# Performance work log

Hardware: AMD Instinct MI355X
Metric: run time of the kernel (lower is better)

## Reference

```python
import jax, jax.numpy as jnp
import numpy as np

# Module constants (match init_kwargs / DCNv4 defaults)
N, C, H, W = 4, 256, 128, 128
G = 4                       # DCNv4 default group
KS = 3                      # kernel_size
K = KS * KS                 # 9 sampling points per group
Cg = C // G                 # channels per group
PAD_OFF = int(np.ceil(G * K * 3 / 8) * 8)  # 112, padded offset_mask dim
EPS = 1e-5                  # BatchNorm2d eps


def setup_inputs() -> dict:
    key = jax.random.key(0)
    ks = jax.random.split(key, 6)
    s = 0.05
    return {
        "x": jax.random.normal(ks[0], (N, C, H, W), jnp.float32),
        "conv_w": jax.random.normal(ks[1], (C, C, 1, 1), jnp.float32) * s,
        "bn1_gamma": jnp.ones((C,), jnp.float32),
        "bn1_beta": jnp.zeros((C,), jnp.float32),
        "bn1_mean": jnp.zeros((C,), jnp.float32),
        "bn1_var": jnp.ones((C,), jnp.float32),
        "value_w": jax.random.normal(ks[2], (C, C), jnp.float32) * s,
        "value_b": jnp.zeros((C,), jnp.float32),
        "offset_w": jax.random.normal(ks[3], (PAD_OFF, C), jnp.float32) * s,
        "offset_b": jnp.zeros((PAD_OFF,), jnp.float32),
        "out_w": jax.random.normal(ks[4], (C, C), jnp.float32) * s,
        "out_b": jnp.zeros((C,), jnp.float32),
        "bn2_gamma": jnp.ones((C,), jnp.float32),
        "bn2_beta": jnp.zeros((C,), jnp.float32),
        "bn2_mean": jnp.zeros((C,), jnp.float32),
        "bn2_var": jnp.ones((C,), jnp.float32),
    }


def _bilinear(v, lh, lw):
    """Bilinear sample v:(N,H,W,G,Cg) at float locs lh/lw:(N,H,W,G); zero outside."""
    n, h, w, g, c = v.shape
    h0 = jnp.floor(lh)
    w0 = jnp.floor(lw)
    dh = lh - h0
    dw = lw - w0
    h0i = h0.astype(jnp.int32)
    w0i = w0.astype(jnp.int32)
    vf = v.reshape(n, h * w, g, c)

    def gather(hh, ww):
        valid = (hh >= 0) & (hh < h) & (ww >= 0) & (ww < w)
        idx = jnp.clip(hh, 0, h - 1) * w + jnp.clip(ww, 0, w - 1)
        out = jnp.take_along_axis(vf, idx.reshape(n, h * w, g)[..., None], axis=1)
        return out.reshape(n, h, w, g, c) * valid[..., None].astype(v.dtype)

    w00 = (1 - dh) * (1 - dw)
    w01 = (1 - dh) * dw
    w10 = dh * (1 - dw)
    w11 = dh * dw
    return (gather(h0i, w0i) * w00[..., None]
            + gather(h0i, w0i + 1) * w01[..., None]
            + gather(h0i + 1, w0i) * w10[..., None]
            + gather(h0i + 1, w0i + 1) * w11[..., None])


def _bn(x_nchw, gamma, beta, mean, var):
    scale = (gamma / jnp.sqrt(var + EPS))[None, :, None, None]
    return x_nchw * scale + (beta - mean * gamma / jnp.sqrt(var + EPS))[None, :, None, None]


def reference(x, conv_w, bn1_gamma, bn1_beta, bn1_mean, bn1_var,
              value_w, value_b, offset_w, offset_b, out_w, out_b,
              bn2_gamma, bn2_beta, bn2_mean, bn2_var):
    n, _, h, w = x.shape
    # ---- Conv(c1,c2,k=1): 1x1 conv (no bias) + BN + SiLU ----
    y = jnp.einsum('nchw,oc->nohw', x, conv_w[:, :, 0, 0])
    y = jax.nn.silu(_bn(y, bn1_gamma, bn1_beta, bn1_mean, bn1_var))

    # ---- DCNv4 on (N, L, C) tokens ----
    t = y.transpose(0, 2, 3, 1)                      # (N,H,W,C)
    v = t @ value_w.T + value_b                      # value_proj
    om = t @ offset_w.T + offset_b                   # (N,H,W,112)
    om = om[..., : G * K * 3].reshape(n, h, w, G, K * 3)
    off = om[..., : 2 * K].reshape(n, h, w, G, K, 2) # (dx, dy) per point
    mask = om[..., 2 * K:]                           # (N,H,W,G,K), no softmax in v4
    v = v.reshape(n, h, w, G, Cg)

    hi = jnp.arange(h, dtype=jnp.float32)[None, :, None, None]
    wi = jnp.arange(w, dtype=jnp.float32)[None, None, :, None]
    out = jnp.zeros_like(v)
    for k in range(K):  # fixed small kernel loop (9 points)
        i, j = divmod(k, KS)
        lh = hi + (i - 1) + off[..., k, 1]           # stride=1, pad=1, dil=1
        lw = wi + (j - 1) + off[..., k, 0]           # offset_scale=1.0
        out = out + mask[..., k, None] * _bilinear(v, lh, lw)

    o = out.reshape(n, h, w, C) @ out_w.T + out_b    # output_proj
    o = o.transpose(0, 3, 1, 2)                      # back to NCHW

    # ---- final BN + SiLU ----
    return jax.nn.silu(_bn(o, bn2_gamma, bn2_beta, bn2_mean, bn2_var))
```

## Files before the change

### kernel.cpp

```cpp
#include <hip/hip_runtime.h>
#include <cstdint>

typedef unsigned short u16;
typedef unsigned int   u32;
typedef __attribute__((ext_vector_type(8))) __bf16 bf16x8;
typedef __attribute__((ext_vector_type(4))) float  f32x4;
typedef __attribute__((ext_vector_type(4))) u32    u32x4;

#define N_IMG 4
#define C_DIM 256
#define H_DIM 128
#define W_DIM 128
#define HW    (H_DIM * W_DIM)
#define M_TOT (N_IMG * HW)
#define CG    64
#define PADOFF 112
#define EPSV  1e-5f

__device__ __forceinline__ u16 f2b(float f) {
  u32 u = __float_as_uint(f);
  u += 0x7fffu + ((u >> 16) & 1u);
  return (u16)(u >> 16);
}

__device__ __forceinline__ void async_cp16(const void* g, void* l) {
  __builtin_amdgcn_global_load_lds(
      (const __attribute__((address_space(1))) void*)g,
      (__attribute__((address_space(3))) void*)l, 16, 0, 0);
}

__global__ __launch_bounds__(256) void cast_all(
    const float* __restrict__ a0, u16* __restrict__ o0,
    const float* __restrict__ a1, u16* __restrict__ o1,
    const float* __restrict__ a2, u16* __restrict__ o2,
    const float* __restrict__ a3, u16* __restrict__ o3) {
  int i = blockIdx.x * 256 + threadIdx.x;
  const float* in; u16* out; int base;
  if (i < 16384)      { in = a0; out = o0; base = 0; }
  else if (i < 32768) { in = a1; out = o1; base = 16384; }
  else if (i < 39936) { in = a2; out = o2; base = 32768; }
  else                { in = a3; out = o3; base = 39936; }
  int j = i - base;
  f32x4 v = reinterpret_cast<const f32x4*>(in)[j];
  u32 lo = (u32)f2b(v[0]) | ((u32)f2b(v[1]) << 16);
  u32 hi = (u32)f2b(v[2]) | ((u32)f2b(v[3]) << 16);
  reinterpret_cast<u32*>(out)[2 * j]     = lo;
  reinterpret_cast<u32*>(out)[2 * j + 1] = hi;
}

__global__ __launch_bounds__(256) void nchw_to_nhwc(const float* __restrict__ in,
                                                    u16* __restrict__ out) {
  __shared__ float tile[64][65];
  const int z = blockIdx.z;
  in  += (size_t)z * C_DIM * HW;
  out += (size_t)z * HW * C_DIM;
  const int p0 = blockIdx.x * 64;
  const int c0 = blockIdx.y * 64;
  const int t = threadIdx.x;
  const int col = t & 63, rb = t >> 6;
#pragma unroll
  for (int i = 0; i < 16; ++i) {
    int row = rb + i * 4;
    tile[row][col] = in[(size_t)(c0 + row) * HW + p0 + col];
  }
  __syncthreads();
  const int cp = t & 31, pb = t >> 5;
#pragma unroll
  for (int i = 0; i < 8; ++i) {
    int p = pb + i * 8;
    u32 pk = (u32)f2b(tile[2 * cp][p]) | ((u32)f2b(tile[2 * cp + 1][p]) << 16);
    *reinterpret_cast<u32*>(out + (size_t)(p0 + p) * C_DIM + c0 + 2 * cp) = pk;
  }
}

template <int MODE>
__global__ __launch_bounds__(256) void gemm_ep(
    const u16* __restrict__ A, const u16* __restrict__ B,
    u16* __restrict__ Cb, float* __restrict__ Cf, int K, int Nreal,
    const float* __restrict__ bias, const float* __restrict__ bias2,
    const float* __restrict__ gamma, const float* __restrict__ beta,
    const float* __restrict__ mean, const float* __restrict__ var) {
  constexpr int BM = 128, BK = 64;
  __shared__ __align__(16) u16 As[BM * BK];
  __shared__ __align__(16) u16 Bs[BM * BK];
  const int tid  = threadIdx.x;
  const int lane = tid & 63;
  const int wave = tid >> 6;
  const int quad = lane >> 4;
  const int l16  = lane & 15;
  const int bm = blockIdx.x * BM;
  const int bn = blockIdx.y * BM;
  const int wm = (wave & 1) * 64;
  const int wn = (wave >> 1) * 64;

  f32x4 acc[4][4] = {};

  for (int ko = 0; ko < K; ko += BK) {
#pragma unroll
    for (int it = 0; it < 4; ++it) {
      int chunk = it * 256 + tid;
      int r  = chunk >> 3;
      int j  = chunk & 7;
      int kk = (j ^ (r & 7)) << 3;
      const u16* ga = A + (size_t)(bm + r) * K + (ko + kk);
      int br = bn + r; if (br >= Nreal) br = Nreal - 1;
      const u16* gb = B + (size_t)br * K + (ko + kk);
      u16* la = As + (size_t)(it * 256 + wave * 64) * 8;
      u16* lb = Bs + (size_t)(it * 256 + wave * 64) * 8;
      async_cp16(ga, la);
      async_cp16(gb, lb);
    }
    __syncthreads();
    const bf16x8* Ap = reinterpret_cast<const bf16x8*>(As);
    const bf16x8* Bp = reinterpret_cast<const bf16x8*>(Bs);
#pragma unroll
    for (int ks = 0; ks < 2; ++ks) {
      bf16x8 af[4], bfr[4];
#pragma unroll
      for (int mi = 0; mi < 4; ++mi) {
        int row = wm + mi * 16 + l16;
        af[mi] = Ap[row * 8 + ((ks * 4 + quad) ^ (row & 7))];
      }
#pragma unroll
      for (int ni = 0; ni < 4; ++ni) {
        int row = wn + ni * 16 + l16;
        bfr[ni] = Bp[row * 8 + ((ks * 4 + quad) ^ (row & 7))];
      }
#pragma unroll
      for (int mi = 0; mi < 4; ++mi)
#pragma unroll
        for (int ni = 0; ni < 4; ++ni)
          acc[mi][ni] = __builtin_amdgcn_mfma_f32_16x16x32_bf16(
              af[mi], bfr[ni], acc[mi][ni], 0, 0, 0);
    }
    __syncthreads();
  }

#pragma unroll
  for (int ni = 0; ni < 4; ++ni) {
    int n = bn + wn + ni * 16 + l16;
    if constexpr (MODE == 0) {
      float sc = gamma[n] * rsqrtf(var[n] + EPSV);
      float sh = beta[n] - mean[n] * sc;
#pragma unroll
      for (int mi = 0; mi < 4; ++mi) {
        int mrow = bm + wm + mi * 16 + quad * 4;
#pragma unroll
        for (int i = 0; i < 4; ++i) {
          float y = acc[mi][ni][i] * sc + sh;
          y = y / (1.f + __expf(-y));
          Cb[(size_t)(mrow + i) * C_DIM + n] = f2b(y);
        }
      }
    } else if constexpr (MODE == 3) {
      float sc = gamma[n] * rsqrtf(var[n] + EPSV);
      float sh = beta[n] - mean[n] * sc + bias[n] * sc;
#pragma unroll
      for (int mi = 0; mi < 4; ++mi) {
        int mrow = bm + wm + mi * 16 + quad * 4;
        int img = mrow >> 14;
        int hw  = mrow & (HW - 1);
        f32x4 y;
#pragma unroll
        for (int i = 0; i < 4; ++i) {
          float z = acc[mi][ni][i] * sc + sh;
          y[i] = z / (1.f + __expf(-z));
        }
        *reinterpret_cast<f32x4*>(
            Cf + (size_t)img * C_DIM * HW + (size_t)n * HW + hw) = y;
      }
    } else {
      if (bn < C_DIM) {
        float sh = bias[n];
#pragma unroll
        for (int mi = 0; mi < 4; ++mi) {
          int mrow = bm + wm + mi * 16 + quad * 4;
#pragma unroll
          for (int i = 0; i < 4; ++i)
            Cb[(size_t)(mrow + i) * C_DIM + n] = f2b(acc[mi][ni][i] + sh);
        }
      } else {
        int col = n - C_DIM;
        bool ok = col < PADOFF;
        float sh = ok ? bias2[col] : 0.f;
#pragma unroll
        for (int mi = 0; mi < 4; ++mi) {
          int mrow = bm + wm + mi * 16 + quad * 4;
#pragma unroll
          for (int i = 0; i < 4; ++i)
            if (ok) Cf[(size_t)(mrow + i) * PADOFF + col] = acc[mi][ni][i] + sh;
        }
      }
    }
  }
}

__global__ __launch_bounds__(256) void dcn_sample(
    const u16* __restrict__ v, const float* __restrict__ om,
    u16* __restrict__ outp) {
  __shared__ float sm[16 * PADOFF];
  const int tid = threadIdx.x;
  const int bid = blockIdx.x;
  const int cpx = gridDim.x >> 3;
  const int wg  = (bid & 7) * cpx + (bid >> 3);
  const int m0  = wg * 16;
  {
    const float* src = om + (size_t)m0 * PADOFF;
#pragma unroll
    for (int i = 0; i < 7; ++i) sm[tid + i * 256] = src[tid + i * 256];
  }
  __syncthreads();
  const int c4 = tid & 3;
  const int g  = (tid >> 2) & 3;
  const int pl = tid >> 4;
  const int m  = m0 + pl;
  const int n  = m >> 14;
  const int hw = m & (HW - 1);
  const int h = hw >> 7, w = hw & 127;
  const float* p = sm + pl * PADOFF + g * 27;
  const u16* vb = v + (size_t)n * HW * C_DIM + g * CG + c4 * 16;
  float acc[16] = {};
#pragma unroll
  for (int k = 0; k < 9; ++k) {
    const int di = k / 3 - 1, dj = k % 3 - 1;
    float ox = p[2 * k], oy = p[2 * k + 1], mk = p[18 + k];
    float lh = (float)(h + di) + oy;
    float lw = (float)(w + dj) + ox;
    float fh = floorf(lh), fw = floorf(lw);
    float dh = lh - fh, dw = lw - fw;
    int h0 = (int)fh, w0 = (int)fw;
    float wy0 = (1.f - dh) * mk, wy1 = dh * mk;
    float wx0 = 1.f - dw, wx1 = dw;
    bool okw0 = (u32)w0 < (u32)W_DIM;
    bool okw1 = (u32)(w0 + 1) < (u32)W_DIM;
    int w0c = min(max(w0, 0), W_DIM - 1);
    int w1c = min(max(w0 + 1, 0), W_DIM - 1);
#pragma unroll
    for (int cy = 0; cy < 2; ++cy) {
      int hh = h0 + cy;
      bool okh = (u32)hh < (u32)H_DIM;
      int hc = min(max(hh, 0), H_DIM - 1);
      const u16* rowp = vb + (size_t)(hc << 7) * C_DIM;
      const u16* qA = rowp + (size_t)w0c * C_DIM;
      const u16* qB = rowp + (size_t)w1c * C_DIM;
      u32x4 a0 = *reinterpret_cast<const u32x4*>(qA);
      u32x4 a1 = *reinterpret_cast<const u32x4*>(qA + 8);
      u32x4 b0 = *reinterpret_cast<const u32x4*>(qB);
      u32x4 b1 = *reinterpret_cast<const u32x4*>(qB + 8);
      float wyc = (cy == 0) ? wy0 : wy1;
      float wtA = (okh && okw0) ? wyc * wx0 : 0.f;
      float wtB = (okh && okw1) ? wyc * wx1 : 0.f;
      u32 wp;
      asm("v_cvt_pk_bf16_f32 %0, %1, %2" : "=v"(wp) : "v"(wtA), "v"(wtB));
#pragma unroll
      for (int j = 0; j < 4; ++j) {
        u32 lo0 = __builtin_amdgcn_perm(a0[j], b0[j], 0x01000504u);
        u32 hi0 = __builtin_amdgcn_perm(a0[j], b0[j], 0x03020706u);
        u32 lo1 = __builtin_amdgcn_perm(a1[j], b1[j], 0x01000504u);
        u32 hi1 = __builtin_amdgcn_perm(a1[j], b1[j], 0x03020706u);
        asm("v_dot2_f32_bf16 %0, %1, %2, %3"
            : "=v"(acc[2 * j]) : "v"(lo0), "v"(wp), "v"(acc[2 * j]));
        asm("v_dot2_f32_bf16 %0, %1, %2, %3"
            : "=v"(acc[2 * j + 1]) : "v"(hi0), "v"(wp), "v"(acc[2 * j + 1]));
        asm("v_dot2_f32_bf16 %0, %1, %2, %3"
            : "=v"(acc[8 + 2 * j]) : "v"(lo1), "v"(wp), "v"(acc[8 + 2 * j]));
        asm("v_dot2_f32_bf16 %0, %1, %2, %3"
            : "=v"(acc[8 + 2 * j + 1]) : "v"(hi1), "v"(wp), "v"(acc[8 + 2 * j + 1]));
      }
    }
  }
  u32x4 r0, r1;
#pragma unroll
  for (int j = 0; j < 4; ++j) {
    u32 pa, pb;
    asm("v_cvt_pk_bf16_f32 %0, %1, %2"
        : "=v"(pa) : "v"(acc[2 * j]), "v"(acc[2 * j + 1]));
    asm("v_cvt_pk_bf16_f32 %0, %1, %2"
        : "=v"(pb) : "v"(acc[8 + 2 * j]), "v"(acc[8 + 2 * j + 1]));
    r0[j] = pa; r1[j] = pb;
  }
  u16* o = outp + (size_t)m * C_DIM + g * CG + c4 * 16;
  *reinterpret_cast<u32x4*>(o)     = r0;
  *reinterpret_cast<u32x4*>(o + 8) = r1;
}

extern "C" void kernel_launch(void* const* d_in, const int* in_sizes, int n_in,
                              void* d_out, int out_size, void* d_ws, size_t ws_size,
                              hipStream_t stream) {
  const float* x        = (const float*)d_in[0];
  const float* conv_w   = (const float*)d_in[1];
  const float* bn1_g    = (const float*)d_in[2];
  const float* bn1_b    = (const float*)d_in[3];
  const float* bn1_m    = (const float*)d_in[4];
  const float* bn1_v    = (const float*)d_in[5];
  const float* value_w  = (const float*)d_in[6];
  const float* value_b  = (const float*)d_in[7];
  const float* offset_w = (const float*)d_in[8];
  const float* offset_b = (const float*)d_in[9];
  const float* out_w    = (const float*)d_in[10];
  const float* out_b    = (const float*)d_in[11];
  const float* bn2_g    = (const float*)d_in[12];
  const float* bn2_b    = (const float*)d_in[13];
  const float* bn2_m    = (const float*)d_in[14];
  const float* bn2_v    = (const float*)d_in[15];

  char* ws = (char*)d_ws;
  u16*   xt   = (u16*)(ws);
  u16*   t    = (u16*)(ws + 33554432);
  u16*   vv   = (u16*)(ws + 67108864);
  float* om   = (float*)(ws + 100663296);
  u16*   wc   = (u16*)(ws + 130023424);
  u16*   wcat = (u16*)(ws + 130154496);
  u16*   wout = (u16*)(ws + 130342912);
  u16*   dcn  = xt;
  float* outp = (float*)d_out;

  cast_all<<<220, 256, 0, stream>>>(conv_w, wc, value_w, wcat,
                                    offset_w, wcat + 65536, out_w, wout);

  nchw_to_nhwc<<<dim3(HW / 64, C_DIM / 64, N_IMG), 256, 0, stream>>>(x, xt);
  gemm_ep<0><<<dim3(M_TOT / 128, 2), 256, 0, stream>>>(
      xt, wc, t, nullptr, C_DIM, C_DIM,
      nullptr, nullptr, bn1_g, bn1_b, bn1_m, bn1_v);
  gemm_ep<1><<<dim3(M_TOT / 128, 3), 256, 0, stream>>>(
      t, wcat, vv, om, C_DIM, C_DIM + PADOFF,
      value_b, offset_b, nullptr, nullptr, nullptr, nullptr);
  dcn_sample<<<dim3(M_TOT / 16), 256, 0, stream>>>(vv, om, dcn);
  gemm_ep<3><<<dim3(M_TOT / 128, 2), 256, 0, stream>>>(
      dcn, wout, nullptr, outp, C_DIM, C_DIM,
      out_b, nullptr, bn2_g, bn2_b, bn2_m, bn2_v);
}
```

Baseline: 278.7 us.

## Fuse NCHW-to-NHWC transpose and bf16 cast into first conv GEMM

Drops the separate nchw_to_nhwc kernel and adds a gemm_conv kernel that reads the fp32 NCHW input directly, converts it to bf16 in registers and writes a swizzled A tile into shared memory, then runs the 1x1-conv MFMA GEMM with the BN+SiLU epilogue. This removes one full write and read of the transposed activation tensor plus a kernel launch. In exchange the K tile shrinks to 32, the A loads are strided fp32 with synchronous staging rather than async copies, and since both N-blocks read the input, the fp32 input is read twice.

```diff
diff --git a/kernel.cpp b/kernel.cpp
--- a/kernel.cpp
+++ b/kernel.cpp
@@ -4,6 +4,7 @@
 typedef unsigned short u16;
 typedef unsigned int   u32;
 typedef __attribute__((ext_vector_type(8))) __bf16 bf16x8;
+typedef __attribute__((ext_vector_type(2))) float  f32x2;
 typedef __attribute__((ext_vector_type(4))) float  f32x4;
 typedef __attribute__((ext_vector_type(4))) u32    u32x4;
 
@@ -48,28 +49,95 @@
   reinterpret_cast<u32*>(out)[2 * j + 1] = hi;
 }
 
-__global__ __launch_bounds__(256) void nchw_to_nhwc(const float* __restrict__ in,
-                                                    u16* __restrict__ out) {
-  __shared__ float tile[64][65];
-  const int z = blockIdx.z;
-  in  += (size_t)z * C_DIM * HW;
-  out += (size_t)z * HW * C_DIM;
-  const int p0 = blockIdx.x * 64;
-  const int c0 = blockIdx.y * 64;
-  const int t = threadIdx.x;
-  const int col = t & 63, rb = t >> 6;
-#pragma unroll
-  for (int i = 0; i < 16; ++i) {
-    int row = rb + i * 4;
-    tile[row][col] = in[(size_t)(c0 + row) * HW + p0 + col];
-  }
-  __syncthreads();
-  const int cp = t & 31, pb = t >> 5;
-#pragma unroll
-  for (int i = 0; i < 8; ++i) {
-    int p = pb + i * 8;
-    u32 pk = (u32)f2b(tile[2 * cp][p]) | ((u32)f2b(tile[2 * cp + 1][p]) << 16);
-    *reinterpret_cast<u32*>(out + (size_t)(p0 + p) * C_DIM + c0 + 2 * cp) = pk;
+__global__ __launch_bounds__(256) void gemm_conv(
+    const float* __restrict__ X, const u16* __restrict__ B,
+    u16* __restrict__ Cb,
+    const float* __restrict__ gamma, const float* __restrict__ beta,
+    const float* __restrict__ mean, const float* __restrict__ var) {
+  constexpr int BM = 128, BK = 32;
+  __shared__ __align__(16) u16 As[BM * BK];
+  __shared__ __align__(16) u16 Bs[BM * BK];
+  const int tid  = threadIdx.x;
+  const int lane = tid & 63;
+  const int wave = tid >> 6;
+  const int quad = lane >> 4;
+  const int l16  = lane & 15;
+  const int bm = blockIdx.x * BM;
+  const int bn = blockIdx.y * BM;
+  const int wm = (wave & 1) * 64;
+  const int wn = (wave >> 1) * 64;
+  const int img = bm >> 14;
+  const int hw0 = bm & (HW - 1);
+  const int p2  = (tid & 63) * 2;
+  const int hh  = tid >> 6;
+  const float* xb = X + (size_t)img * C_DIM * HW + hw0 + p2;
+
+  f32x4 acc[4][4] = {};
+
+  for (int ko = 0; ko < C_DIM; ko += BK) {
+    float a0[8], a1[8];
+#pragma unroll
+    for (int j = 0; j < 8; ++j) {
+      f32x2 fv = *reinterpret_cast<const f32x2*>(
+          xb + (size_t)(ko + hh * 8 + j) * HW);
+      a0[j] = fv.x; a1[j] = fv.y;
+    }
+    u32x4 w0, w1;
+#pragma unroll
+    for (int j = 0; j < 4; ++j) {
+      w0[j] = (u32)f2b(a0[2 * j]) | ((u32)f2b(a0[2 * j + 1]) << 16);
+      w1[j] = (u32)f2b(a1[2 * j]) | ((u32)f2b(a1[2 * j + 1]) << 16);
+    }
+    {
+      u32x4* Ar = reinterpret_cast<u32x4*>(As);
+      int sw = hh ^ ((p2 >> 1) & 3);
+      Ar[p2 * 4 + sw]       = w0;
+      Ar[(p2 + 1) * 4 + sw] = w1;
+    }
+#pragma unroll
+    for (int it = 0; it < 2; ++it) {
+      int chunk = it * 256 + tid;
+      int r  = chunk >> 2;
+      int kk = (chunk & 3) << 3;
+      async_cp16(B + (size_t)(bn + r) * C_DIM + (ko + kk),
+                 Bs + (size_t)(it * 256 + wave * 64) * 8);
+    }
+    __syncthreads();
+    const bf16x8* Apf = reinterpret_cast<const bf16x8*>(As);
+    const bf16x8* Bpf = reinterpret_cast<const bf16x8*>(Bs);
+    bf16x8 af[4], bfr[4];
+#pragma unroll
+    for (int mi = 0; mi < 4; ++mi) {
+      int r = wm + mi * 16 + l16;
+      af[mi] = Apf[r * 4 + (quad ^ ((r >> 1) & 3))];
+    }
+#pragma unroll
+    for (int ni = 0; ni < 4; ++ni)
+      bfr[ni] = Bpf[(wn + ni * 16 + l16) * 4 + quad];
+#pragma unroll
+    for (int mi = 0; mi < 4; ++mi)
+#pragma unroll
+      for (int ni = 0; ni < 4; ++ni)
+        acc[mi][ni] = __builtin_amdgcn_mfma_f32_16x16x32_bf16(
+            af[mi], bfr[ni], acc[mi][ni], 0, 0, 0);
+    __syncthreads();
+  }
+
+#pragma unroll
+  for (int ni = 0; ni < 4; ++ni) {
+    int n = bn + wn + ni * 16 + l16;
+    float sc = gamma[n] * rsqrtf(var[n] + EPSV);
+    float sh = beta[n] - mean[n] * sc;
+#pragma unroll
+    for (int mi = 0; mi < 4; ++mi) {
+      int mrow = bm + wm + mi * 16 + quad * 4;
+#pragma unroll
+      for (int i = 0; i < 4; ++i) {
+        float y = acc[mi][ni][i] * sc + sh;
+        y = y / (1.f + __expf(-y));
+        Cb[(size_t)(mrow + i) * C_DIM + n] = f2b(y);
+      }
+    }
   }
 }
 
@@ -139,20 +207,7 @@
 #pragma unroll
   for (int ni = 0; ni < 4; ++ni) {
     int n = bn + wn + ni * 16 + l16;
-    if constexpr (MODE == 0) {
-      float sc = gamma[n] * rsqrtf(var[n] + EPSV);
-      float sh = beta[n] - mean[n] * sc;
-#pragma unroll
-      for (int mi = 0; mi < 4; ++mi) {
-        int mrow = bm + wm + mi * 16 + quad * 4;
-#pragma unroll
-        for (int i = 0; i < 4; ++i) {
-          float y = acc[mi][ni][i] * sc + sh;
-          y = y / (1.f + __expf(-y));
-          Cb[(size_t)(mrow + i) * C_DIM + n] = f2b(y);
-        }
-      }
-    } else if constexpr (MODE == 3) {
+    if constexpr (MODE == 3) {
       float sc = gamma[n] * rsqrtf(var[n] + EPSV);
       float sh = beta[n] - mean[n] * sc + bias[n] * sc;
 #pragma unroll
@@ -305,23 +360,20 @@
   const float* bn2_v    = (const float*)d_in[15];
 
   char* ws = (char*)d_ws;
-  u16*   xt   = (u16*)(ws);
+  u16*   dcn  = (u16*)(ws);
   u16*   t    = (u16*)(ws + 33554432);
   u16*   vv   = (u16*)(ws + 67108864);
   float* om   = (float*)(ws + 100663296);
   u16*   wc   = (u16*)(ws + 130023424);
   u16*   wcat = (u16*)(ws + 130154496);
   u16*   wout = (u16*)(ws + 130342912);
-  u16*   dcn  = xt;
   float* outp = (float*)d_out;
 
   cast_all<<<220, 256, 0, stream>>>(conv_w, wc, value_w, wcat,
                                     offset_w, wcat + 65536, out_w, wout);
 
-  nchw_to_nhwc<<<dim3(HW / 64, C_DIM / 64, N_IMG), 256, 0, stream>>>(x, xt);
-  gemm_ep<0><<<dim3(M_TOT / 128, 2), 256, 0, stream>>>(
-      xt, wc, t, nullptr, C_DIM, C_DIM,
-      nullptr, nullptr, bn1_g, bn1_b, bn1_m, bn1_v);
+  gemm_conv<<<dim3(M_TOT / 128, 2), 256, 0, stream>>>(
+      x, wc, t, bn1_g, bn1_b, bn1_m, bn1_v);
   gemm_ep<1><<<dim3(M_TOT / 128, 3), 256, 0, stream>>>(
       t, wcat, vv, om, C_DIM, C_DIM + PADOFF,
       value_b, offset_b, nullptr, nullptr, nullptr, nullptr);
```

New measurement: 270.0 us. 3.1% less time.
